# Performance work log

Hardware: AMD Instinct MI355X
Metric: run time of the kernel (lower is better)

The kernel has to match this reference:

```python
import jax, jax.numpy as jnp
import numpy as np

B, S, D, H = 2, 4096, 512, 8
DK = D // H
LN_EPS = 1e-5


def setup_inputs() -> dict:
    key = jax.random.key(0)
    ks = jax.random.split(key, 12)
    lim = 1.0 / np.sqrt(D)
    inp = {
        "query": jax.random.normal(ks[0], (B, S, D), jnp.float32),
        "key_in": jax.random.normal(ks[1], (B, S, D), jnp.float32),
        "value": jax.random.normal(ks[2], (B, S, D), jnp.float32),
        # causal mask: positions with 0 are masked out (masked_fill(mask == 0, -1e9))
        "mask": jnp.broadcast_to(jnp.tril(jnp.ones((S, S), jnp.int32)), (B, S, S)),
        "Wq": jax.random.uniform(ks[3], (D, D), jnp.float32, -lim, lim),
        "bq": jnp.zeros((D,), jnp.float32),
        "Wk": jax.random.uniform(ks[4], (D, D), jnp.float32, -lim, lim),
        "bk": jnp.zeros((D,), jnp.float32),
        "Wv": jax.random.uniform(ks[5], (D, D), jnp.float32, -lim, lim),
        "bv": jnp.zeros((D,), jnp.float32),
        "Wo": jax.random.uniform(ks[6], (D, D), jnp.float32, -lim, lim),
        "bo": jnp.zeros((D,), jnp.float32),
        "ln_gamma": jnp.ones((D,), jnp.float32),
        "ln_beta": jnp.zeros((D,), jnp.float32),
    }
    return inp


def _split_heads(x):
    # [B, S, D] -> [B, H, S, DK]
    return x.reshape(B, S, H, DK).transpose(0, 2, 1, 3)


def reference(query, key_in, value, mask, Wq, bq, Wk, bk, Wv, bv, Wo, bo, ln_gamma, ln_beta):
    residual = query
    q = _split_heads(query @ Wq.T + bq)
    k = _split_heads(key_in @ Wk.T + bk)
    v = _split_heads(value @ Wv.T + bv)

    scores = jnp.einsum("bhqd,bhkd->bhqk", q, k) / jnp.sqrt(jnp.float32(DK))
    scores = jnp.where(mask[:, None, :, :] == 0, jnp.float32(-1e9), scores)
    attn = jax.nn.softmax(scores, axis=-1)  # dropout is identity in eval mode
    out = jnp.einsum("bhqk,bhkd->bhqd", attn, v)

    out = out.transpose(0, 2, 1, 3).reshape(B, S, D)
    out = out @ Wo.T + bo

    x = out + residual
    mu = jnp.mean(x, axis=-1, keepdims=True)
    var = jnp.mean(jnp.square(x - mu), axis=-1, keepdims=True)
    return (x - mu) * jax.lax.rsqrt(var + LN_EPS) * ln_gamma + ln_beta
```

## Files before the change

### kernel.cpp

```cpp
#include <hip/hip_runtime.h>
#include <hip/hip_bf16.h>

#define B_ 2
#define S_ 4096
#define D_ 512
#define H_ 8
#define DK_ 64

typedef short short8_t __attribute__((ext_vector_type(8)));
typedef short short4_t __attribute__((ext_vector_type(4)));
typedef float float4_t __attribute__((ext_vector_type(4)));

__device__ __forceinline__ short f2bf(float f) {
    union { float f; unsigned u; } c; c.f = f;
    unsigned r = c.u + 0x7FFFu + ((c.u >> 16) & 1u);
    return (short)(r >> 16);
}

#define MFMA32(a, b, c) __builtin_amdgcn_mfma_f32_16x16x32_bf16((a), (b), (c), 0, 0, 0)

#if __has_builtin(__builtin_amdgcn_mfma_f32_16x16x16bf16_1k)
__device__ __forceinline__ float4_t MFMA16(short4_t a, short4_t b, float4_t c) {
    return __builtin_amdgcn_mfma_f32_16x16x16bf16_1k(a, b, c, 0, 0, 0);
}
#else
__device__ __forceinline__ float4_t MFMA16(short4_t a, short4_t b, float4_t c) {
    asm volatile("v_mfma_f32_16x16x16_bf16 %0, %1, %2, %0" : "+v"(c) : "v"(a), "v"(b));
    return c;
}
#endif

__device__ __forceinline__ void gll16(const void* g, const void* l) {
    __builtin_amdgcn_global_load_lds(
        (__attribute__((address_space(1))) void*)(g),
        (__attribute__((address_space(3))) void*)(l), 16, 0, 0);
}

__global__ __launch_bounds__(256) void convert_all(
    const float* __restrict__ q, const float* __restrict__ k, const float* __restrict__ v,
    const float* __restrict__ Wq, const float* __restrict__ Wk,
    const float* __restrict__ Wv, const float* __restrict__ Wo,
    short* __restrict__ Xq, short* __restrict__ Xk, short* __restrict__ Xv,
    short* __restrict__ Wbf)
{
    const int XN = (B_ * S_ * D_) / 8;
    int gid = blockIdx.x * 256 + threadIdx.x;
    const float* src;
    short8_t* dst;
    int off;
    if (gid < 3 * XN) {
        int z = gid >> 19;
        off = gid & (XN - 1);
        src = (z == 0) ? q : (z == 1) ? k : v;
        dst = (short8_t*)((z == 0) ? Xq : (z == 1) ? Xk : Xv);
    } else {
        int g2 = gid - 3 * XN;
        int z = g2 >> 15;
        off = g2 & 32767;
        src = (z == 0) ? Wq : (z == 1) ? Wk : (z == 2) ? Wv : Wo;
        dst = (short8_t*)(Wbf + z * (D_ * D_));
    }
    float4_t f0 = ((const float4_t*)src)[off * 2];
    float4_t f1 = ((const float4_t*)src)[off * 2 + 1];
    short8_t o = { f2bf(f0[0]), f2bf(f0[1]), f2bf(f0[2]), f2bf(f0[3]),
                   f2bf(f1[0]), f2bf(f1[1]), f2bf(f1[2]), f2bf(f1[3]) };
    dst[off] = o;
}

__global__ __launch_bounds__(256) void gemm_qkv(
    const short* __restrict__ Xq, const short* __restrict__ Xk, const short* __restrict__ Xv,
    const short* __restrict__ Wbf,
    const float* __restrict__ bq, const float* __restrict__ bk, const float* __restrict__ bv,
    short* __restrict__ Qs, short* __restrict__ Ks, short* __restrict__ Vt)
{
    __shared__ short sA[128 * 64];
    __shared__ short sB[128 * 64];

    const int z = blockIdx.z;
    const short* X    = (z == 0) ? Xq : (z == 1) ? Xk : Xv;
    const short* W    = Wbf + z * (D_ * D_);
    const float* bias = (z == 0) ? bq : (z == 1) ? bk : bv;

    const int col0 = blockIdx.x * 128, row0 = blockIdx.y * 128;
    const int tid = threadIdx.x, w = tid >> 6, l = tid & 63;
    const int lr = l & 15, lg = l >> 4;
    const int wm = w >> 1, wn = w & 1;
    const int srow = l >> 3, sch = l & 7;

    float4_t acc[4][4];
    #pragma unroll
    for (int i = 0; i < 4; i++)
        #pragma unroll
        for (int j = 0; j < 4; j++)
            acc[i][j] = (float4_t){0.f, 0.f, 0.f, 0.f};

    for (int k0 = 0; k0 < D_; k0 += 64) {
        #pragma unroll
        for (int rnd = 0; rnd < 4; rnd++) {
            int r = rnd * 32 + w * 8 + srow;
            gll16(X + (row0 + r) * D_ + k0 + (sch ^ (r & 7)) * 8, &sA[(rnd * 32 + w * 8) * 64]);
            gll16(W + (col0 + r) * D_ + k0 + (sch ^ (r & 7)) * 8, &sB[(rnd * 32 + w * 8) * 64]);
        }
        __syncthreads();
        #pragma unroll
        for (int kk = 0; kk < 2; kk++) {
            short8_t a[4], bb[4];
            #pragma unroll
            for (int i = 0; i < 4; i++) {
                int rw = wm * 64 + i * 16 + lr;
                a[i] = *(const short8_t*)(&sA[rw * 64 + (((kk * 4 + lg) ^ (lr & 7)) * 8)]);
            }
            #pragma unroll
            for (int j = 0; j < 4; j++) {
                int rw = wn * 64 + j * 16 + lr;
                bb[j] = *(const short8_t*)(&sB[rw * 64 + (((kk * 4 + lg) ^ (lr & 7)) * 8)]);
            }
            #pragma unroll
            for (int i = 0; i < 4; i++)
                #pragma unroll
                for (int j = 0; j < 4; j++)
                    acc[i][j] = MFMA32(a[i], bb[j], acc[i][j]);
        }
        __syncthreads();
    }

    if (z < 2) {
        short* Out = (z == 0) ? Qs : Ks;
        #pragma unroll
        for (int j = 0; j < 4; j++) {
            int col = col0 + wn * 64 + j * 16 + lr;
            float bv_ = bias[col];
            int h = col >> 6, dk = col & 63;
            #pragma unroll
            for (int i = 0; i < 4; i++) {
                int gm0 = row0 + wm * 64 + i * 16 + lg * 4;
                #pragma unroll
                for (int r = 0; r < 4; r++) {
                    int gm = gm0 + r;
                    Out[(((gm >> 12) * H_ + h) * S_ + (gm & 4095)) * 64 + dk] =
                        f2bf(acc[i][j][r] + bv_);
                }
            }
        }
    } else {
        #pragma unroll
        for (int j = 0; j < 4; j++) {
            int col = col0 + wn * 64 + j * 16 + lr;
            float bv_ = bias[col];
            int h = col >> 6, dk = col & 63;
            #pragma unroll
            for (int i = 0; i < 4; i++) {
                int gm0 = row0 + wm * 64 + i * 16 + lg * 4;
                int bidx = gm0 >> 12;
                int tl = (gm0 >> 6) & 63;
                short4_t o4 = { f2bf(acc[i][j][0] + bv_), f2bf(acc[i][j][1] + bv_),
                                f2bf(acc[i][j][2] + bv_), f2bf(acc[i][j][3] + bv_) };
                *(short4_t*)(Vt + ((bidx * H_ + h) * 64 + dk) * S_ + tl * 64 + lg * 16 + i * 4) = o4;
            }
        }
    }
}

__global__ __launch_bounds__(256) void attn_kernel(
    const short* __restrict__ Qs, const short* __restrict__ Ks,
    const short* __restrict__ Vt, short* __restrict__ Og)
{
    __shared__ short sK[2][64 * 64];
    __shared__ short sV[2][64 * 64];

    const int bh = blockIdx.y, b = bh >> 3, h = bh & 7;
    const int qt = (int)gridDim.x - 1 - (int)blockIdx.x;
    const int tid = threadIdx.x, w = tid >> 6, l = tid & 63;
    const int lr = l & 15, lg = l >> 4;
    const int qbase = qt * 128 + w * 32;
    const int kvT = 2 * qt + 2;
    const int myT = (qbase + 31) / 64 + 1;
    const short* Kb = Ks + bh * (S_ * 64);
    const short* Vb = Vt + bh * (64 * S_);
    const int srow = l >> 3, sch = l & 7;

    short8_t qf[2][2];
    #pragma unroll
    for (int qb = 0; qb < 2; qb++)
        #pragma unroll
        for (int kk = 0; kk < 2; kk++)
            qf[qb][kk] = *(const short8_t*)(Qs + bh * (S_ * 64) +
                                            (qbase + qb * 16 + lr) * 64 + kk * 32 + lg * 8);

    float m_run[2] = {-1e30f, -1e30f}, l_run[2] = {0.f, 0.f};
    float4_t O[2][4];
    #pragma unroll
    for (int qb = 0; qb < 2; qb++)
        #pragma unroll
        for (int nj = 0; nj < 4; nj++)
            O[qb][nj] = (float4_t){0.f, 0.f, 0.f, 0.f};

    auto STAGE = [&](int t, int bi) {
        #pragma unroll
        for (int rnd = 0; rnd < 2; rnd++) {
            int r = rnd * 32 + w * 8 + srow;
            gll16(Kb + (t * 64 + r) * 64 + (sch ^ (r & 7)) * 8, &sK[bi][(rnd * 32 + w * 8) * 64]);
            gll16(Vb + r * S_ + t * 64 + (sch ^ (r & 7)) * 8,   &sV[bi][(rnd * 32 + w * 8) * 64]);
        }
    };

    STAGE(0, 0);
    for (int t = 0; t < kvT; t++) {
        int cur = t & 1;
        if (t + 1 < kvT) {
            STAGE(t + 1, cur ^ 1);
            asm volatile("s_waitcnt vmcnt(4)" ::: "memory");
        } else {
            asm volatile("s_waitcnt vmcnt(0)" ::: "memory");
        }
        __builtin_amdgcn_s_barrier();
        __builtin_amdgcn_sched_barrier(0);

        if (t < myT) {
            const short* K_ = sK[cur];
            const short* V_ = sV[cur];

            float4_t st[2][4];
            #pragma unroll
            for (int qb = 0; qb < 2; qb++)
                #pragma unroll
                for (int nj = 0; nj < 4; nj++)
                    st[qb][nj] = (float4_t){0.f, 0.f, 0.f, 0.f};
            #pragma unroll
            for (int kk = 0; kk < 2; kk++)
                #pragma unroll
                for (int nj = 0; nj < 4; nj++) {
                    short8_t kf = *(const short8_t*)(&K_[(nj * 16 + lr) * 64 +
                                                         (((kk * 4 + lg) ^ (lr & 7)) * 8)]);
                    st[0][nj] = MFMA32(kf, qf[0][kk], st[0][nj]);
                    st[1][nj] = MFMA32(kf, qf[1][kk], st[1][nj]);
                }

            short4_t pb[2][4];
            #pragma unroll
            for (int qb = 0; qb < 2; qb++) {
                int qg = qbase + qb * 16 + lr;
                bool mm = (t * 64 + 63 > qbase + qb * 16);
                float sv[4][4];
                #pragma unroll
                for (int nj = 0; nj < 4; nj++)
                    #pragma unroll
                    for (int r = 0; r < 4; r++) {
                        float vv = st[qb][nj][r] * 0.125f;
                        if (mm) {
                            int kvg = t * 64 + nj * 16 + lg * 4 + r;
                            if (kvg > qg) vv = -1e30f;
                        }
                        sv[nj][r] = vv;
                    }
                float mx = sv[0][0];
                #pragma unroll
                for (int nj = 0; nj < 4; nj++)
                    #pragma unroll
                    for (int r = 0; r < 4; r++) mx = fmaxf(mx, sv[nj][r]);
                mx = fmaxf(mx, __shfl_xor(mx, 16));
                mx = fmaxf(mx, __shfl_xor(mx, 32));
                float mnew = fmaxf(m_run[qb], mx);
                float al = __expf(m_run[qb] - mnew);
                m_run[qb] = mnew;
                float rs = 0.f;
                #pragma unroll
                for (int nj = 0; nj < 4; nj++)
                    #pragma unroll
                    for (int r = 0; r < 4; r++) {
                        float e = __expf(sv[nj][r] - mnew);
                        sv[nj][r] = e;
                        rs += e;
                    }
                rs += __shfl_xor(rs, 16);
                rs += __shfl_xor(rs, 32);
                l_run[qb] = l_run[qb] * al + rs;
                #pragma unroll
                for (int nj = 0; nj < 4; nj++) O[qb][nj] *= al;
                #pragma unroll
                for (int nj = 0; nj < 4; nj++)
                    pb[qb][nj] = (short4_t){ f2bf(sv[nj][0]), f2bf(sv[nj][1]),
                                             f2bf(sv[nj][2]), f2bf(sv[nj][3]) };
            }

            #pragma unroll
            for (int njd = 0; njd < 4; njd++) {
                const short* vr = &V_[(njd * 16 + lr) * 64];
                short8_t v0 = *(const short8_t*)(vr + (((lg * 2)     ^ (lr & 7)) * 8));
                short8_t v1 = *(const short8_t*)(vr + (((lg * 2 + 1) ^ (lr & 7)) * 8));
                short4_t va0 = __builtin_shufflevector(v0, v0, 0, 1, 2, 3);
                short4_t va1 = __builtin_shufflevector(v0, v0, 4, 5, 6, 7);
                short4_t va2 = __builtin_shufflevector(v1, v1, 0, 1, 2, 3);
                short4_t va3 = __builtin_shufflevector(v1, v1, 4, 5, 6, 7);
                #pragma unroll
                for (int qb = 0; qb < 2; qb++) {
                    O[qb][njd] = MFMA16(va0, pb[qb][0], O[qb][njd]);
                    O[qb][njd] = MFMA16(va1, pb[qb][1], O[qb][njd]);
                    O[qb][njd] = MFMA16(va2, pb[qb][2], O[qb][njd]);
                    O[qb][njd] = MFMA16(va3, pb[qb][3], O[qb][njd]);
                }
            }
        }
        __builtin_amdgcn_s_barrier();
        __builtin_amdgcn_sched_barrier(0);
    }

    #pragma unroll
    for (int qb = 0; qb < 2; qb++) {
        float inv = 1.f / l_run[qb];
        int qg = qbase + qb * 16 + lr;
        #pragma unroll
        for (int njd = 0; njd < 4; njd++) {
            short4_t o4 = { f2bf(O[qb][njd][0] * inv), f2bf(O[qb][njd][1] * inv),
                            f2bf(O[qb][njd][2] * inv), f2bf(O[qb][njd][3] * inv) };
            *(short4_t*)(Og + (b * S_ + qg) * D_ + h * 64 + njd * 16 + lg * 4) = o4;
        }
    }
}

__global__ __launch_bounds__(256) void gemm_oproj(
    const short* __restrict__ Ag, const short* __restrict__ Wbf,
    const float* __restrict__ bo, float* __restrict__ Og)
{
    __shared__ short sA[128 * 64];
    __shared__ short sB[128 * 64];

    const int col0 = blockIdx.x * 128, row0 = blockIdx.y * 128;
    const int tid = threadIdx.x, w = tid >> 6, l = tid & 63;
    const int lr = l & 15, lg = l >> 4;
    const int wm = w >> 1, wn = w & 1;
    const int srow = l >> 3, sch = l & 7;

    float4_t acc[4][4];
    #pragma unroll
    for (int i = 0; i < 4; i++)
        #pragma unroll
        for (int j = 0; j < 4; j++)
            acc[i][j] = (float4_t){0.f, 0.f, 0.f, 0.f};

    for (int k0 = 0; k0 < D_; k0 += 64) {
        #pragma unroll
        for (int rnd = 0; rnd < 4; rnd++) {
            int r = rnd * 32 + w * 8 + srow;
            gll16(Ag  + (row0 + r) * D_ + k0 + (sch ^ (r & 7)) * 8, &sA[(rnd * 32 + w * 8) * 64]);
            gll16(Wbf + (col0 + r) * D_ + k0 + (sch ^ (r & 7)) * 8, &sB[(rnd * 32 + w * 8) * 64]);
        }
        __syncthreads();
        #pragma unroll
        for (int kk = 0; kk < 2; kk++) {
            short8_t a[4], bb[4];
            #pragma unroll
            for (int i = 0; i < 4; i++) {
                int rw = wm * 64 + i * 16 + lr;
                a[i] = *(const short8_t*)(&sA[rw * 64 + (((kk * 4 + lg) ^ (lr & 7)) * 8)]);
            }
            #pragma unroll
            for (int j = 0; j < 4; j++) {
                int rw = wn * 64 + j * 16 + lr;
                bb[j] = *(const short8_t*)(&sB[rw * 64 + (((kk * 4 + lg) ^ (lr & 7)) * 8)]);
            }
            #pragma unroll
            for (int i = 0; i < 4; i++)
                #pragma unroll
                for (int j = 0; j < 4; j++)
                    acc[i][j] = MFMA32(a[i], bb[j], acc[i][j]);
        }
        __syncthreads();
    }

    #pragma unroll
    for (int j = 0; j < 4; j++) {
        int col = col0 + wn * 64 + j * 16 + lr;
        float bv_ = bo[col];
        #pragma unroll
        for (int i = 0; i < 4; i++) {
            int gm0 = row0 + wm * 64 + i * 16 + lg * 4;
            #pragma unroll
            for (int r = 0; r < 4; r++)
                Og[(gm0 + r) * D_ + col] = acc[i][j][r] + bv_;
        }
    }
}

__global__ __launch_bounds__(128) void ln_kernel(
    const float* __restrict__ Oin, const float* __restrict__ resid,
    const float* __restrict__ gamma, const float* __restrict__ beta,
    float* __restrict__ out)
{
    __shared__ float red[4];
    const int row = blockIdx.x, tid = threadIdx.x;
    float4_t o  = *(const float4_t*)(Oin   + row * 512 + tid * 4);
    float4_t rq = *(const float4_t*)(resid + row * 512 + tid * 4);
    float4_t x = o + rq;
    float s1 = x[0] + x[1] + x[2] + x[3];
    float s2 = x[0]*x[0] + x[1]*x[1] + x[2]*x[2] + x[3]*x[3];
    #pragma unroll
    for (int m = 1; m < 64; m <<= 1) {
        s1 += __shfl_xor(s1, m, 64);
        s2 += __shfl_xor(s2, m, 64);
    }
    const int wv = tid >> 6;
    if ((tid & 63) == 0) { red[wv * 2] = s1; red[wv * 2 + 1] = s2; }
    __syncthreads();
    s1 = red[0] + red[2];
    s2 = red[1] + red[3];
    float mu  = s1 * (1.f / 512.f);
    float var = s2 * (1.f / 512.f) - mu * mu;
    float rstd = rsqrtf(var + 1e-5f);
    float4_t g  = *(const float4_t*)(gamma + tid * 4);
    float4_t be = *(const float4_t*)(beta  + tid * 4);
    float4_t y;
    #pragma unroll
    for (int c = 0; c < 4; c++) y[c] = (x[c] - mu) * rstd * g[c] + be[c];
    *(float4_t*)(out + row * 512 + tid * 4) = y;
}

extern "C" void kernel_launch(void* const* d_in, const int* in_sizes, int n_in,
                              void* d_out, int out_size, void* d_ws, size_t ws_size,
                              hipStream_t stream) {
    const float* q     = (const float*)d_in[0];
    const float* kin   = (const float*)d_in[1];
    const float* vin   = (const float*)d_in[2];
    const float* Wq    = (const float*)d_in[4];
    const float* bq    = (const float*)d_in[5];
    const float* Wk    = (const float*)d_in[6];
    const float* bk    = (const float*)d_in[7];
    const float* Wv    = (const float*)d_in[8];
    const float* bv    = (const float*)d_in[9];
    const float* Wo    = (const float*)d_in[10];
    const float* bo    = (const float*)d_in[11];
    const float* gamma = (const float*)d_in[12];
    const float* beta  = (const float*)d_in[13];
    float* out = (float*)d_out;

    char* ws = (char*)d_ws;
    short* Wbf  = (short*)(ws);
    short* Xq   = (short*)(ws + 2097152);
    short* Xk   = (short*)(ws + 10485760);
    short* Xv   = (short*)(ws + 18874368);
    short* Qs   = (short*)(ws + 27262976);
    short* Ks   = (short*)(ws + 35651584);
    short* Vt   = (short*)(ws + 44040192);
    short* Attn = (short*)(ws + 18874368);
    float* Oprj = (float*)(ws + 2097152);

    convert_all<<<6656, 256, 0, stream>>>(q, kin, vin, Wq, Wk, Wv, Wo, Xq, Xk, Xv, Wbf);
    gemm_qkv<<<dim3(4, 64, 3), 256, 0, stream>>>(Xq, Xk, Xv, Wbf, bq, bk, bv, Qs, Ks, Vt);
    attn_kernel<<<dim3(32, 16), 256, 0, stream>>>(Qs, Ks, Vt, Attn);
    gemm_oproj<<<dim3(4, 64), 256, 0, stream>>>(Attn, Wbf + 3 * D_ * D_, bo, Oprj);
    ln_kernel<<<8192, 128, 0, stream>>>(Oprj, q, gamma, beta, out);
}
```

Before: 432.0 us.

## Split attention KV across waves with LDS merge; vectorize GEMM epilogues via operand swap

The attention kernel now gives each block 32 queries instead of 128 and launches 2048 blocks with a swizzled head/tile mapping. The four waves split each 64-key tile, one 16-key slice per wave, and their partial softmax states and outputs are merged through LDS at the end. Softmax switches to exp2 with a folded log2 scale and uses s_setprio around the MFMA sections. The QKV and output-projection GEMMs swap MFMA operands so the accumulator layout allows vectorized bias loads and short4/float4 stores; the V transposed store also changes its sequence layout. This trades a larger grid and the extra merge/LDS traffic for better load balance and coalesced epilogue writes.

```diff
diff --git a/kernel.cpp b/kernel.cpp
--- a/kernel.cpp
+++ b/kernel.cpp
@@ -102,9 +102,9 @@
             gll16(W + (col0 + r) * D_ + k0 + (sch ^ (r & 7)) * 8, &sB[(rnd * 32 + w * 8) * 64]);
         }
         __syncthreads();
+        short8_t a[4], bb[4];
         #pragma unroll
         for (int kk = 0; kk < 2; kk++) {
-            short8_t a[4], bb[4];
             #pragma unroll
             for (int i = 0; i < 4; i++) {
                 int rw = wm * 64 + i * 16 + lr;
@@ -115,11 +115,19 @@
                 int rw = wn * 64 + j * 16 + lr;
                 bb[j] = *(const short8_t*)(&sB[rw * 64 + (((kk * 4 + lg) ^ (lr & 7)) * 8)]);
             }
-            #pragma unroll
-            for (int i = 0; i < 4; i++)
-                #pragma unroll
-                for (int j = 0; j < 4; j++)
-                    acc[i][j] = MFMA32(a[i], bb[j], acc[i][j]);
+            if (z < 2) {
+                #pragma unroll
+                for (int i = 0; i < 4; i++)
+                    #pragma unroll
+                    for (int j = 0; j < 4; j++)
+                        acc[i][j] = MFMA32(bb[j], a[i], acc[i][j]);
+            } else {
+                #pragma unroll
+                for (int i = 0; i < 4; i++)
+                    #pragma unroll
+                    for (int j = 0; j < 4; j++)
+                        acc[i][j] = MFMA32(a[i], bb[j], acc[i][j]);
+            }
         }
         __syncthreads();
     }
@@ -128,55 +136,55 @@
         short* Out = (z == 0) ? Qs : Ks;
         #pragma unroll
         for (int j = 0; j < 4; j++) {
-            int col = col0 + wn * 64 + j * 16 + lr;
-            float bv_ = bias[col];
-            int h = col >> 6, dk = col & 63;
+            int colb = col0 + wn * 64 + j * 16 + lg * 4;
+            int h = colb >> 6, dk = colb & 63;
+            float4_t b4 = *(const float4_t*)(bias + colb);
             #pragma unroll
             for (int i = 0; i < 4; i++) {
-                int gm0 = row0 + wm * 64 + i * 16 + lg * 4;
-                #pragma unroll
-                for (int r = 0; r < 4; r++) {
-                    int gm = gm0 + r;
-                    Out[(((gm >> 12) * H_ + h) * S_ + (gm & 4095)) * 64 + dk] =
-                        f2bf(acc[i][j][r] + bv_);
-                }
+                int s = row0 + wm * 64 + i * 16 + lr;
+                short4_t o4 = { f2bf(acc[i][j][0] + b4[0]), f2bf(acc[i][j][1] + b4[1]),
+                                f2bf(acc[i][j][2] + b4[2]), f2bf(acc[i][j][3] + b4[3]) };
+                *(short4_t*)(Out + (((s >> 12) * H_ + h) * S_ + (s & 4095)) * 64 + dk) = o4;
             }
         }
     } else {
         #pragma unroll
         for (int j = 0; j < 4; j++) {
-            int col = col0 + wn * 64 + j * 16 + lr;
-            float bv_ = bias[col];
-            int h = col >> 6, dk = col & 63;
+            int dkg = col0 + wn * 64 + j * 16 + lr;
+            int h = dkg >> 6, dk = dkg & 63;
+            float bv_ = bias[dkg];
             #pragma unroll
             for (int i = 0; i < 4; i++) {
-                int gm0 = row0 + wm * 64 + i * 16 + lg * 4;
-                int bidx = gm0 >> 12;
-                int tl = (gm0 >> 6) & 63;
+                int s0 = row0 + wm * 64 + i * 16 + lg * 4;
                 short4_t o4 = { f2bf(acc[i][j][0] + bv_), f2bf(acc[i][j][1] + bv_),
                                 f2bf(acc[i][j][2] + bv_), f2bf(acc[i][j][3] + bv_) };
-                *(short4_t*)(Vt + ((bidx * H_ + h) * 64 + dk) * S_ + tl * 64 + lg * 16 + i * 4) = o4;
-            }
-        }
-    }
-}
+                *(short4_t*)(Vt + (((s0 >> 12) * H_ + h) * 64 + dk) * S_ + (s0 & 4095)) = o4;
+            }
+        }
+    }
+}
+
+#define SCALE_LOG2 0.1803368801111244f
 
 __global__ __launch_bounds__(256) void attn_kernel(
     const short* __restrict__ Qs, const short* __restrict__ Ks,
     const short* __restrict__ Vt, short* __restrict__ Og)
 {
-    __shared__ short sK[2][64 * 64];
-    __shared__ short sV[2][64 * 64];
-
-    const int bh = blockIdx.y, b = bh >> 3, h = bh & 7;
-    const int qt = (int)gridDim.x - 1 - (int)blockIdx.x;
+    __shared__ float smem[8192];
+    short* sKb = (short*)smem;
+    short* sVb = (short*)smem + 8192;
+
+    const int v = blockIdx.x;
+    const int bh = (v & 7) * 2 + ((v >> 3) & 1);
+    const int qt = 127 - (v >> 4);
+    const int b = bh >> 3, h = bh & 7;
     const int tid = threadIdx.x, w = tid >> 6, l = tid & 63;
     const int lr = l & 15, lg = l >> 4;
-    const int qbase = qt * 128 + w * 32;
-    const int kvT = 2 * qt + 2;
-    const int myT = (qbase + 31) / 64 + 1;
+    const int qbase = qt * 32;
+    const int kvT = qt / 2 + 1;
     const short* Kb = Ks + bh * (S_ * 64);
     const short* Vb = Vt + bh * (64 * S_);
+    const short* Qb = Qs + bh * (S_ * 64);
     const int srow = l >> 3, sch = l & 7;
 
     short8_t qf[2][2];
@@ -184,8 +192,7 @@
     for (int qb = 0; qb < 2; qb++)
         #pragma unroll
         for (int kk = 0; kk < 2; kk++)
-            qf[qb][kk] = *(const short8_t*)(Qs + bh * (S_ * 64) +
-                                            (qbase + qb * 16 + lr) * 64 + kk * 32 + lg * 8);
+            qf[qb][kk] = *(const short8_t*)(Qb + (qbase + qb * 16 + lr) * 64 + kk * 32 + lg * 8);
 
     float m_run[2] = {-1e30f, -1e30f}, l_run[2] = {0.f, 0.f};
     float4_t O[2][4];
@@ -199,8 +206,8 @@
         #pragma unroll
         for (int rnd = 0; rnd < 2; rnd++) {
             int r = rnd * 32 + w * 8 + srow;
-            gll16(Kb + (t * 64 + r) * 64 + (sch ^ (r & 7)) * 8, &sK[bi][(rnd * 32 + w * 8) * 64]);
-            gll16(Vb + r * S_ + t * 64 + (sch ^ (r & 7)) * 8,   &sV[bi][(rnd * 32 + w * 8) * 64]);
+            gll16(Kb + (t * 64 + r) * 64 + (sch ^ (r & 7)) * 8, sKb + bi * 4096 + (rnd * 32 + w * 8) * 64);
+            gll16(Vb + r * S_ + t * 64 + (sch ^ (r & 7)) * 8,   sVb + bi * 4096 + (rnd * 32 + w * 8) * 64);
         }
     };
 
@@ -216,105 +223,126 @@
         __builtin_amdgcn_s_barrier();
         __builtin_amdgcn_sched_barrier(0);
 
-        if (t < myT) {
-            const short* K_ = sK[cur];
-            const short* V_ = sV[cur];
-
-            float4_t st[2][4];
-            #pragma unroll
-            for (int qb = 0; qb < 2; qb++)
-                #pragma unroll
-                for (int nj = 0; nj < 4; nj++)
-                    st[qb][nj] = (float4_t){0.f, 0.f, 0.f, 0.f};
+        const int kv0 = t * 64 + w * 16;
+        if (kv0 <= qbase + 16) {
+            const short* K_ = sKb + cur * 4096;
+            const short* V_ = sVb + cur * 4096;
+
+            short8_t kf[2];
             #pragma unroll
             for (int kk = 0; kk < 2; kk++)
-                #pragma unroll
-                for (int nj = 0; nj < 4; nj++) {
-                    short8_t kf = *(const short8_t*)(&K_[(nj * 16 + lr) * 64 +
-                                                         (((kk * 4 + lg) ^ (lr & 7)) * 8)]);
-                    st[0][nj] = MFMA32(kf, qf[0][kk], st[0][nj]);
-                    st[1][nj] = MFMA32(kf, qf[1][kk], st[1][nj]);
+                kf[kk] = *(const short8_t*)(&K_[(w * 16 + lr) * 64 + (((kk * 4 + lg) ^ (lr & 7)) * 8)]);
+
+            __builtin_amdgcn_s_setprio(1);
+            float4_t st0 = (float4_t){0.f, 0.f, 0.f, 0.f}, st1 = st0;
+            st0 = MFMA32(kf[0], qf[0][0], st0);
+            st1 = MFMA32(kf[0], qf[1][0], st1);
+            st0 = MFMA32(kf[1], qf[0][1], st0);
+            st1 = MFMA32(kf[1], qf[1][1], st1);
+            __builtin_amdgcn_s_setprio(0);
+
+            const bool act0 = (kv0 <= qbase);
+            const bool diag0 = (kv0 == qbase);
+            const bool diag1 = (kv0 == qbase + 16);
+            short4_t pb[2];
+
+            #pragma unroll
+            for (int qb = 0; qb < 2; qb++) {
+                if (qb == 0 && !act0) continue;
+                float4_t sx = qb ? st1 : st0;
+                bool dg = qb ? diag1 : diag0;
+                float sval[4];
+                #pragma unroll
+                for (int r = 0; r < 4; r++) {
+                    float vv = sx[r] * SCALE_LOG2;
+                    if (dg && (lg * 4 + r > lr)) vv = -1e30f;
+                    sval[r] = vv;
                 }
-
-            short4_t pb[2][4];
-            #pragma unroll
-            for (int qb = 0; qb < 2; qb++) {
-                int qg = qbase + qb * 16 + lr;
-                bool mm = (t * 64 + 63 > qbase + qb * 16);
-                float sv[4][4];
-                #pragma unroll
-                for (int nj = 0; nj < 4; nj++)
-                    #pragma unroll
-                    for (int r = 0; r < 4; r++) {
-                        float vv = st[qb][nj][r] * 0.125f;
-                        if (mm) {
-                            int kvg = t * 64 + nj * 16 + lg * 4 + r;
-                            if (kvg > qg) vv = -1e30f;
-                        }
-                        sv[nj][r] = vv;
-                    }
-                float mx = sv[0][0];
-                #pragma unroll
-                for (int nj = 0; nj < 4; nj++)
-                    #pragma unroll
-                    for (int r = 0; r < 4; r++) mx = fmaxf(mx, sv[nj][r]);
+                float mx = fmaxf(fmaxf(sval[0], sval[1]), fmaxf(sval[2], sval[3]));
                 mx = fmaxf(mx, __shfl_xor(mx, 16));
                 mx = fmaxf(mx, __shfl_xor(mx, 32));
                 float mnew = fmaxf(m_run[qb], mx);
-                float al = __expf(m_run[qb] - mnew);
+                float al = __builtin_exp2f(m_run[qb] - mnew);
                 m_run[qb] = mnew;
                 float rs = 0.f;
                 #pragma unroll
-                for (int nj = 0; nj < 4; nj++)
-                    #pragma unroll
-                    for (int r = 0; r < 4; r++) {
-                        float e = __expf(sv[nj][r] - mnew);
-                        sv[nj][r] = e;
-                        rs += e;
-                    }
+                for (int r = 0; r < 4; r++) {
+                    float e = __builtin_exp2f(sval[r] - mnew);
+                    sval[r] = e;
+                    rs += e;
+                }
                 rs += __shfl_xor(rs, 16);
                 rs += __shfl_xor(rs, 32);
                 l_run[qb] = l_run[qb] * al + rs;
                 #pragma unroll
                 for (int nj = 0; nj < 4; nj++) O[qb][nj] *= al;
-                #pragma unroll
-                for (int nj = 0; nj < 4; nj++)
-                    pb[qb][nj] = (short4_t){ f2bf(sv[nj][0]), f2bf(sv[nj][1]),
-                                             f2bf(sv[nj][2]), f2bf(sv[nj][3]) };
-            }
-
+                pb[qb] = (short4_t){ f2bf(sval[0]), f2bf(sval[1]), f2bf(sval[2]), f2bf(sval[3]) };
+            }
+
+            __builtin_amdgcn_s_setprio(1);
             #pragma unroll
             for (int njd = 0; njd < 4; njd++) {
-                const short* vr = &V_[(njd * 16 + lr) * 64];
-                short8_t v0 = *(const short8_t*)(vr + (((lg * 2)     ^ (lr & 7)) * 8));
-                short8_t v1 = *(const short8_t*)(vr + (((lg * 2 + 1) ^ (lr & 7)) * 8));
-                short4_t va0 = __builtin_shufflevector(v0, v0, 0, 1, 2, 3);
-                short4_t va1 = __builtin_shufflevector(v0, v0, 4, 5, 6, 7);
-                short4_t va2 = __builtin_shufflevector(v1, v1, 0, 1, 2, 3);
-                short4_t va3 = __builtin_shufflevector(v1, v1, 4, 5, 6, 7);
-                #pragma unroll
-                for (int qb = 0; qb < 2; qb++) {
-                    O[qb][njd] = MFMA16(va0, pb[qb][0], O[qb][njd]);
-                    O[qb][njd] = MFMA16(va1, pb[qb][1], O[qb][njd]);
-                    O[qb][njd] = MFMA16(va2, pb[qb][2], O[qb][njd]);
-                    O[qb][njd] = MFMA16(va3, pb[qb][3], O[qb][njd]);
-                }
-            }
+                short4_t va = *(const short4_t*)(
+                    &V_[(njd * 16 + lr) * 64 + (((w * 2 + (lg >> 1)) ^ (lr & 7)) * 8) + (lg & 1) * 4]);
+                if (act0) O[0][njd] = MFMA16(va, pb[0], O[0][njd]);
+                O[1][njd] = MFMA16(va, pb[1], O[1][njd]);
+            }
+            __builtin_amdgcn_s_setprio(0);
         }
         __builtin_amdgcn_s_barrier();
         __builtin_amdgcn_sched_barrier(0);
     }
 
+    float* sml = smem;
+    if (lg == 0) {
+        #pragma unroll
+        for (int qb = 0; qb < 2; qb++) {
+            sml[((w * 2 + qb) * 16 + lr) * 2 + 0] = m_run[qb];
+            sml[((w * 2 + qb) * 16 + lr) * 2 + 1] = l_run[qb];
+        }
+    }
+    __syncthreads();
+    float fac[2];
     #pragma unroll
     for (int qb = 0; qb < 2; qb++) {
-        float inv = 1.f / l_run[qb];
-        int qg = qbase + qb * 16 + lr;
+        float mw[4], lw[4];
+        #pragma unroll
+        for (int ww = 0; ww < 4; ww++) {
+            mw[ww] = sml[((ww * 2 + qb) * 16 + lr) * 2 + 0];
+            lw[ww] = sml[((ww * 2 + qb) * 16 + lr) * 2 + 1];
+        }
+        float mmax = fmaxf(fmaxf(mw[0], mw[1]), fmaxf(mw[2], mw[3]));
+        float lsum = 0.f;
+        #pragma unroll
+        for (int ww = 0; ww < 4; ww++) lsum += __builtin_exp2f(mw[ww] - mmax) * lw[ww];
+        fac[qb] = __builtin_exp2f(m_run[qb] - mmax) / lsum;
+    }
+    __syncthreads();
+    float* rg = smem + w * 2048;
+    #pragma unroll
+    for (int qb = 0; qb < 2; qb++) {
         #pragma unroll
         for (int njd = 0; njd < 4; njd++) {
-            short4_t o4 = { f2bf(O[qb][njd][0] * inv), f2bf(O[qb][njd][1] * inv),
-                            f2bf(O[qb][njd][2] * inv), f2bf(O[qb][njd][3] * inv) };
-            *(short4_t*)(Og + (b * S_ + qg) * D_ + h * 64 + njd * 16 + lg * 4) = o4;
-        }
+            int row = qb * 16 + lr;
+            int c = (njd * 4 + lg) ^ (lr & 7);
+            float4_t val = O[qb][njd] * fac[qb];
+            *(float4_t*)(rg + row * 64 + c * 4) = val;
+        }
+    }
+    __syncthreads();
+    {
+        int qq = tid >> 3, a = tid & 7;
+        int key = qq & 7;
+        float4_t s0 = (float4_t){0.f, 0.f, 0.f, 0.f}, s1 = s0;
+        #pragma unroll
+        for (int ww = 0; ww < 4; ww++) {
+            const float* r_ = smem + ww * 2048 + qq * 64;
+            s0 += *(const float4_t*)(r_ + ((a * 2) ^ key) * 4);
+            s1 += *(const float4_t*)(r_ + ((a * 2 + 1) ^ key) * 4);
+        }
+        short8_t o8 = { f2bf(s0[0]), f2bf(s0[1]), f2bf(s0[2]), f2bf(s0[3]),
+                        f2bf(s1[0]), f2bf(s1[1]), f2bf(s1[2]), f2bf(s1[3]) };
+        *(short8_t*)(Og + (b * S_ + qbase + qq) * D_ + h * 64 + a * 8) = o8;
     }
 }
 
@@ -363,21 +391,20 @@
             for (int i = 0; i < 4; i++)
                 #pragma unroll
                 for (int j = 0; j < 4; j++)
-                    acc[i][j] = MFMA32(a[i], bb[j], acc[i][j]);
+                    acc[i][j] = MFMA32(bb[j], a[i], acc[i][j]);
         }
         __syncthreads();
     }
 
     #pragma unroll
     for (int j = 0; j < 4; j++) {
-        int col = col0 + wn * 64 + j * 16 + lr;
-        float bv_ = bo[col];
+        int colb = col0 + wn * 64 + j * 16 + lg * 4;
+        float4_t b4 = *(const float4_t*)(bo + colb);
         #pragma unroll
         for (int i = 0; i < 4; i++) {
-            int gm0 = row0 + wm * 64 + i * 16 + lg * 4;
-            #pragma unroll
-            for (int r = 0; r < 4; r++)
-                Og[(gm0 + r) * D_ + col] = acc[i][j][r] + bv_;
+            int s = row0 + wm * 64 + i * 16 + lr;
+            float4_t o4 = acc[i][j] + b4;
+            *(float4_t*)(Og + s * D_ + colb) = o4;
         }
     }
 }
@@ -446,7 +473,7 @@
 
     convert_all<<<6656, 256, 0, stream>>>(q, kin, vin, Wq, Wk, Wv, Wo, Xq, Xk, Xv, Wbf);
     gemm_qkv<<<dim3(4, 64, 3), 256, 0, stream>>>(Xq, Xk, Xv, Wbf, bq, bk, bv, Qs, Ks, Vt);
-    attn_kernel<<<dim3(32, 16), 256, 0, stream>>>(Qs, Ks, Vt, Attn);
+    attn_kernel<<<2048, 256, 0, stream>>>(Qs, Ks, Vt, Attn);
     gemm_oproj<<<dim3(4, 64), 256, 0, stream>>>(Attn, Wbf + 3 * D_ * D_, bo, Oprj);
     ln_kernel<<<8192, 128, 0, stream>>>(Oprj, q, gamma, beta, out);
 }
```

After: 418.2 us. 3.2% less time.
